# Kernel tuning notes

Hardware: AMD Instinct MI355X
Metric: run time of the kernel (lower is better)

The kernel has to match this reference:

```python
import jax, jax.numpy as jnp
import numpy as np

B, I, T = 8192, 128, 21
H1, H2, H3 = 256, 256, 128


def _init(key, shape, fan_in):
    # torch-style uniform(-1/sqrt(fan_in), 1/sqrt(fan_in))
    bound = 1.0 / np.sqrt(fan_in)
    return jax.random.uniform(key, shape, jnp.float32, -bound, bound)


def setup_inputs() -> dict:
    key = jax.random.key(0)
    ks = jax.random.split(key, 16)
    x = jax.random.normal(ks[0], (B, I, T), jnp.float32)
    d = {"x": x}
    # stacked LSTM weights (PyTorch layout: W_ih (4H, in), gate order i,f,g,o)
    d["W1_ih"] = _init(ks[1], (4 * H1, I), H1)
    d["b1_ih"] = _init(ks[2], (4 * H1,), H1)
    d["b1_hh"] = _init(ks[3], (4 * H1,), H1)
    d["W2_ih"] = _init(ks[4], (4 * H2, H1), H2)
    d["b2_ih"] = _init(ks[5], (4 * H2,), H2)
    d["b2_hh"] = _init(ks[6], (4 * H2,), H2)
    d["W3_ih"] = _init(ks[7], (4 * H3, H2), H3)
    d["b3_ih"] = _init(ks[8], (4 * H3,), H3)
    d["b3_hh"] = _init(ks[9], (4 * H3,), H3)
    d["fc1_w"] = _init(ks[10], (1, H3), H3)
    d["fc1_b"] = _init(ks[11], (1,), H3)
    d["fc2_w"] = _init(ks[12], (T, T), T)
    d["fc2_b"] = _init(ks[13], (T,), T)
    return d


def _lstm_cell_step(xt, W_ih, b_ih, b_hh):
    # single timestep with h0 = c0 = 0, so the W_hh @ h0 term vanishes
    gates = xt @ W_ih.T + (b_ih + b_hh)          # (B, 21, 4H)
    i, f, g, o = jnp.split(gates, 4, axis=-1)    # torch gate order i,f,g,o
    c = jax.nn.sigmoid(i) * jnp.tanh(g)          # f * c0 = 0
    return jax.nn.sigmoid(o) * jnp.tanh(c)


def reference(x, W1_ih, b1_ih, b1_hh, W2_ih, b2_ih, b2_hh,
              W3_ih, b3_ih, b3_hh, fc1_w, fc1_b, fc2_w, fc2_b):
    # fold the 21 independent single-step columns into the batch dim
    xt = jnp.transpose(x, (0, 2, 1))             # (B, 21, I)
    h1 = _lstm_cell_step(xt, W1_ih, b1_ih, b1_hh)   # (B, 21, H1)
    h2 = _lstm_cell_step(h1, W2_ih, b2_ih, b2_hh)   # (B, 21, H2)
    h3 = _lstm_cell_step(h2, W3_ih, b3_ih, b3_hh)   # (B, 21, H3)
    y = h3 @ fc1_w.T + fc1_b                     # (B, 21, 1)
    y = y[..., 0][:, None, :]                    # (B, 1, 21)  == x_torch
    out = y @ fc2_w.T + fc2_b                    # (B, 1, 21)
    return out
```

## Files before the change

### kernel.cpp

```cpp
#include <hip/hip_runtime.h>
#include <hip/hip_bf16.h>
#include <stdint.h>


typedef __attribute__((ext_vector_type(8))) short bf16x8;
typedef __attribute__((ext_vector_type(4))) float f32x4;

#define M_ROWS 172032
#define BATCH  8192

__device__ __forceinline__ float bf2f(unsigned short u) {
    union { unsigned int i; float f; } v; v.i = ((unsigned int)u) << 16; return v.f;
}
__device__ __forceinline__ unsigned short f2bf(float f) {
    union { float f; unsigned int i; } v; v.f = f;
    unsigned int r = v.i + 0x7fffu + ((v.i >> 16) & 1u);
    return (unsigned short)(r >> 16);
}
__device__ __forceinline__ float sigmoidf_(float x) {
    return __builtin_amdgcn_rcpf(1.0f + __expf(-x));
}
__device__ __forceinline__ float tanhf_(float x) {
    x = fminf(fmaxf(x, -20.0f), 20.0f);
    float e = __expf(-2.0f * x);
    return (1.0f - e) * __builtin_amdgcn_rcpf(1.0f + e);
}

__global__ __launch_bounds__(256) void k_convert(
    const float* __restrict__ src, unsigned short* __restrict__ dst, int n4)
{
    int i = blockIdx.x * 256 + threadIdx.x;
    if (i < n4) {
        float4 v = ((const float4*)src)[i];
        ushort4 o;
        o.x = f2bf(v.x); o.y = f2bf(v.y); o.z = f2bf(v.z); o.w = f2bf(v.w);
        ((ushort4*)dst)[i] = o;
    }
}

__global__ __launch_bounds__(256) void k_transpose(
    const float* __restrict__ x, unsigned short* __restrict__ xt)
{
    __shared__ unsigned short tile[128 * 22];
    const int b = blockIdx.x, tid = threadIdx.x;
    const float* xb = x + (size_t)b * 2688;
    for (int idx = tid; idx < 2688; idx += 256) {
        int i = idx / 21, t = idx - i * 21;
        tile[i * 22 + t] = f2bf(xb[idx]);
    }
    __syncthreads();
    unsigned short* xtb = xt + (size_t)b * 2688;
    for (int idx = tid; idx < 2688; idx += 256) {
        int t = idx >> 7, i = idx & 127;
        xtb[t * 128 + i] = tile[i * 22 + t];
    }
}

template<int K, int HG>
__global__ __launch_bounds__(256, 2) void k_gemm_act(
    const unsigned short* __restrict__ A,
    const unsigned short* __restrict__ W,
    const float* __restrict__ bih,
    const float* __restrict__ bhh,
    unsigned short* __restrict__ Hout)
{
    __shared__ __align__(16) unsigned short As[128 * 64];
    __shared__ __align__(16) unsigned short Ws[192 * 64];
    __shared__ float Bs[192];

    const int tid  = threadIdx.x;
    const int wave = tid >> 6;
    const int lane = tid & 63;
    const int wm = wave >> 1;
    const int wn = wave & 1;
    const int r0 = blockIdx.x * 128;
    const int c0 = blockIdx.y * 64;

    if (tid < 192) {
        int g = tid >> 6, c = tid & 63;
        int gbase = (g == 0) ? 0 : (g + 1) * HG;
        int idx = gbase + c0 + c;
        Bs[tid] = bih[idx] + bhh[idx];
    }

    f32x4 acc[3][4][2];
#pragma unroll
    for (int g = 0; g < 3; ++g)
#pragma unroll
        for (int m = 0; m < 4; ++m)
#pragma unroll
            for (int n = 0; n < 2; ++n)
                acc[g][m][n] = (f32x4){0.f, 0.f, 0.f, 0.f};

#pragma unroll
    for (int kk = 0; kk < K; kk += 64) {
        bf16x8 av[4], wv[6];
#pragma unroll
        for (int i = 0; i < 4; ++i) {
            int q = tid + 256 * i;
            int row = q >> 3, off = (q & 7) * 8;
            av[i] = *(const bf16x8*)(A + (size_t)(r0 + row) * K + kk + off);
        }
#pragma unroll
        for (int i = 0; i < 6; ++i) {
            int q = tid + 256 * i;
            int lrow = q >> 3, off = (q & 7) * 8;
            int gate = lrow >> 6, n = lrow & 63;
            int gbase = (gate == 0) ? 0 : (gate + 1) * HG;
            wv[i] = *(const bf16x8*)(W + (size_t)(gbase + c0 + n) * K + kk + off);
        }
        if (kk) __syncthreads();
#pragma unroll
        for (int i = 0; i < 4; ++i) {
            int q = tid + 256 * i;
            int row = q >> 3, slot = (q & 7) ^ (row & 7);
            *(bf16x8*)&As[row * 64 + slot * 8] = av[i];
        }
#pragma unroll
        for (int i = 0; i < 6; ++i) {
            int q = tid + 256 * i;
            int row = q >> 3, slot = (q & 7) ^ (row & 7);
            *(bf16x8*)&Ws[row * 64 + slot * 8] = wv[i];
        }
        __syncthreads();

#pragma unroll
        for (int ks = 0; ks < 64; ks += 32) {
            bf16x8 af[4];
            bf16x8 bfr[3][2];
            const int rsel = lane & 15;
            const int slot = (ks >> 3) | (lane >> 4);
            const int soff = (slot ^ (rsel & 7)) * 8;
#pragma unroll
            for (int m = 0; m < 4; ++m)
                af[m] = *(const bf16x8*)&As[(wm * 64 + m * 16 + rsel) * 64 + soff];
#pragma unroll
            for (int g = 0; g < 3; ++g)
#pragma unroll
                for (int n = 0; n < 2; ++n)
                    bfr[g][n] = *(const bf16x8*)&Ws[(g * 64 + wn * 32 + n * 16 + rsel) * 64 + soff];
#pragma unroll
            for (int g = 0; g < 3; ++g)
#pragma unroll
                for (int m = 0; m < 4; ++m)
#pragma unroll
                    for (int n = 0; n < 2; ++n)
                        acc[g][m][n] = __builtin_amdgcn_mfma_f32_16x16x32_bf16(
                            af[m], bfr[g][n], acc[g][m][n], 0, 0, 0);
        }
    }

    const int quad = lane >> 4;
    const int csel = lane & 15;
#pragma unroll
    for (int m = 0; m < 4; ++m) {
#pragma unroll
        for (int n = 0; n < 2; ++n) {
            int cloc = wn * 32 + n * 16 + csel;
            float bi = Bs[cloc], bg = Bs[64 + cloc], bo = Bs[128 + cloc];
            f32x4 vi = acc[0][m][n], vg = acc[1][m][n], vo = acc[2][m][n];
#pragma unroll
            for (int r = 0; r < 4; ++r) {
                int row = r0 + wm * 64 + m * 16 + quad * 4 + r;
                float cv = sigmoidf_(vi[r] + bi) * tanhf_(vg[r] + bg);
                float h  = sigmoidf_(vo[r] + bo) * tanhf_(cv);
                Hout[(size_t)row * HG + c0 + cloc] = f2bf(h);
            }
        }
    }
}

#define FSTR 169
__global__ __launch_bounds__(256) void k_final(
    const unsigned short* __restrict__ h3,
    const float* __restrict__ fc1w,
    const float* __restrict__ fc1b,
    const float* __restrict__ fc2w,
    const float* __restrict__ fc2b,
    float* __restrict__ out)
{
    __shared__ unsigned short ht[128 * FSTR];
    __shared__ float fwl[128];
    __shared__ float yl[168];
    __shared__ float f2l[441];
    __shared__ float f2bl[21];

    const int tid = threadIdx.x;
    const int b0 = blockIdx.x * 8;

    if (tid < 128) fwl[tid] = fc1w[tid];
    for (int i = tid; i < 441; i += 256) f2l[i] = fc2w[i];
    if (tid < 21) f2bl[tid] = fc2b[tid];

    const unsigned int* hsrc = (const unsigned int*)(h3 + (size_t)b0 * 2688);
    for (int gi = tid; gi < 10752; gi += 256) {
        unsigned int v = hsrc[gi];
        int e = gi * 2;
        int task = e >> 7;
        int c = e & 127;
        ht[c * FSTR + task] = (unsigned short)(v & 0xffffu);
        ht[(c + 1) * FSTR + task] = (unsigned short)(v >> 16);
    }
    __syncthreads();

    const float f1b = fc1b[0];
    if (tid < 168) {
        float s = f1b;
#pragma unroll 8
        for (int c = 0; c < 128; ++c)
            s += fwl[c] * bf2f(ht[c * FSTR + tid]);
        yl[tid] = s;
    }
    __syncthreads();
    if (tid < 168) {
        int bloc = tid / 21;
        int tp = tid - bloc * 21;
        float s = f2bl[tp];
#pragma unroll
        for (int t = 0; t < 21; ++t)
            s += yl[bloc * 21 + t] * f2l[tp * 21 + t];
        out[(size_t)(b0 + bloc) * 21 + tp] = s;
    }
}

extern "C" void kernel_launch(void* const* d_in, const int* in_sizes, int n_in,
                              void* d_out, int out_size, void* d_ws, size_t ws_size,
                              hipStream_t stream)
{
    const float* x    = (const float*)d_in[0];
    const float* W1   = (const float*)d_in[1];
    const float* b1i  = (const float*)d_in[2];
    const float* b1h  = (const float*)d_in[3];
    const float* W2   = (const float*)d_in[4];
    const float* b2i  = (const float*)d_in[5];
    const float* b2h  = (const float*)d_in[6];
    const float* W3   = (const float*)d_in[7];
    const float* b3i  = (const float*)d_in[8];
    const float* b3h  = (const float*)d_in[9];
    const float* fc1w = (const float*)d_in[10];
    const float* fc1b = (const float*)d_in[11];
    const float* fc2w = (const float*)d_in[12];
    const float* fc2b = (const float*)d_in[13];
    float* out = (float*)d_out;

    unsigned short* Wc1 = (unsigned short*)d_ws;
    unsigned short* Wc2 = Wc1 + 131072;
    unsigned short* Wc3 = Wc2 + 262144;
    unsigned short* buf = Wc3 + 131072;

    int C = 1;
    while (C < 64 && 1048576 + (size_t)(M_ROWS / C) * 1536 > ws_size) C <<= 1;
    const int R  = M_ROWS / C;
    const int Bc = BATCH / C;

    unsigned short* xt = buf;
    unsigned short* h1 = xt + (size_t)R * 128;
    unsigned short* h2 = h1 + (size_t)R * 256;
    unsigned short* h3 = h2 + (size_t)R * 256;

    k_convert<<<128, 256, 0, stream>>>(W1, Wc1, 32768);
    k_convert<<<256, 256, 0, stream>>>(W2, Wc2, 65536);
    k_convert<<<128, 256, 0, stream>>>(W3, Wc3, 32768);

    for (int c = 0; c < C; ++c) {
        const float* xc = x + (size_t)c * Bc * 2688;
        k_transpose<<<Bc, 256, 0, stream>>>(xc, xt);
        k_gemm_act<128, 256><<<dim3(R / 128, 4), 256, 0, stream>>>(xt, Wc1, b1i, b1h, h1);
        k_gemm_act<256, 256><<<dim3(R / 128, 4), 256, 0, stream>>>(h1, Wc2, b2i, b2h, h2);
        k_gemm_act<256, 128><<<dim3(R / 128, 2), 256, 0, stream>>>(h2, Wc3, b3i, b3h, h3);
        k_final<<<Bc / 8, 256, 0, stream>>>(h3, fc1w, fc1b, fc2w, fc2b,
                                            out + (size_t)c * Bc * 21);
    }
}
```

Measured before the change: 421.5 us.

## Load GEMM tiles directly into LDS via global_load_lds and swap grid order

```diff
diff --git a/kernel.cpp b/kernel.cpp
--- a/kernel.cpp
+++ b/kernel.cpp
@@ -24,6 +24,13 @@
     x = fminf(fmaxf(x, -20.0f), 20.0f);
     float e = __expf(-2.0f * x);
     return (1.0f - e) * __builtin_amdgcn_rcpf(1.0f + e);
+}
+
+__device__ __forceinline__ void gload_lds16(const unsigned short* g, unsigned short* l) {
+    __builtin_amdgcn_global_load_lds(
+        (const __attribute__((address_space(1))) unsigned int*)g,
+        (__attribute__((address_space(3))) unsigned int*)l,
+        16, 0, 0);
 }
 
 __global__ __launch_bounds__(256) void k_convert(
@@ -57,7 +64,7 @@
 }
 
 template<int K, int HG>
-__global__ __launch_bounds__(256, 2) void k_gemm_act(
+__global__ __launch_bounds__(256, 3) void k_gemm_act(
     const unsigned short* __restrict__ A,
     const unsigned short* __restrict__ W,
     const float* __restrict__ bih,
@@ -73,8 +80,27 @@
     const int lane = tid & 63;
     const int wm = wave >> 1;
     const int wn = wave & 1;
-    const int r0 = blockIdx.x * 128;
-    const int c0 = blockIdx.y * 64;
+    const int c0 = blockIdx.x * 64;
+    const int r0 = blockIdx.y * 128;
+
+    const unsigned short* aptr[4];
+#pragma unroll
+    for (int i = 0; i < 4; ++i) {
+        int q16 = (wave * 4 + i) * 64 + lane;
+        int row = q16 >> 3, pslot = q16 & 7;
+        int lslot = pslot ^ (row & 7);
+        aptr[i] = A + (size_t)(r0 + row) * K + lslot * 8;
+    }
+    const unsigned short* wptr[6];
+#pragma unroll
+    for (int i = 0; i < 6; ++i) {
+        int q16 = (wave * 6 + i) * 64 + lane;
+        int lrow = q16 >> 3, pslot = q16 & 7;
+        int lslot = pslot ^ (lrow & 7);
+        int gate = lrow >> 6, n = lrow & 63;
+        int gbase = (gate == 0) ? 0 : (gate + 1) * HG;
+        wptr[i] = W + (size_t)(gbase + c0 + n) * K + lslot * 8;
+    }
 
     if (tid < 192) {
         int g = tid >> 6, c = tid & 63;
@@ -94,34 +120,13 @@
 
 #pragma unroll
     for (int kk = 0; kk < K; kk += 64) {
-        bf16x8 av[4], wv[6];
-#pragma unroll
-        for (int i = 0; i < 4; ++i) {
-            int q = tid + 256 * i;
-            int row = q >> 3, off = (q & 7) * 8;
-            av[i] = *(const bf16x8*)(A + (size_t)(r0 + row) * K + kk + off);
-        }
-#pragma unroll
-        for (int i = 0; i < 6; ++i) {
-            int q = tid + 256 * i;
-            int lrow = q >> 3, off = (q & 7) * 8;
-            int gate = lrow >> 6, n = lrow & 63;
-            int gbase = (gate == 0) ? 0 : (gate + 1) * HG;
-            wv[i] = *(const bf16x8*)(W + (size_t)(gbase + c0 + n) * K + kk + off);
-        }
         if (kk) __syncthreads();
 #pragma unroll
-        for (int i = 0; i < 4; ++i) {
-            int q = tid + 256 * i;
-            int row = q >> 3, slot = (q & 7) ^ (row & 7);
-            *(bf16x8*)&As[row * 64 + slot * 8] = av[i];
-        }
-#pragma unroll
-        for (int i = 0; i < 6; ++i) {
-            int q = tid + 256 * i;
-            int row = q >> 3, slot = (q & 7) ^ (row & 7);
-            *(bf16x8*)&Ws[row * 64 + slot * 8] = wv[i];
-        }
+        for (int i = 0; i < 4; ++i)
+            gload_lds16(aptr[i] + kk, &As[(wave * 4 + i) * 512]);
+#pragma unroll
+        for (int i = 0; i < 6; ++i)
+            gload_lds16(wptr[i] + kk, &Ws[(wave * 6 + i) * 512]);
         __syncthreads();
 
 #pragma unroll
@@ -265,9 +270,9 @@
     for (int c = 0; c < C; ++c) {
         const float* xc = x + (size_t)c * Bc * 2688;
         k_transpose<<<Bc, 256, 0, stream>>>(xc, xt);
-        k_gemm_act<128, 256><<<dim3(R / 128, 4), 256, 0, stream>>>(xt, Wc1, b1i, b1h, h1);
-        k_gemm_act<256, 256><<<dim3(R / 128, 4), 256, 0, stream>>>(h1, Wc2, b2i, b2h, h2);
-        k_gemm_act<256, 128><<<dim3(R / 128, 2), 256, 0, stream>>>(h2, Wc3, b3i, b3h, h3);
+        k_gemm_act<128, 256><<<dim3(4, R / 128), 256, 0, stream>>>(xt, Wc1, b1i, b1h, h1);
+        k_gemm_act<256, 256><<<dim3(4, R / 128), 256, 0, stream>>>(h1, Wc2, b2i, b2h, h2);
+        k_gemm_act<256, 128><<<dim3(2, R / 128), 256, 0, stream>>>(h2, Wc3, b3i, b3h, h3);
         k_final<<<Bc / 8, 256, 0, stream>>>(h3, fc1w, fc1b, fc2w, fc2b,
                                             out + (size_t)c * Bc * 21);
     }
```

Result: slower. 435.6 us (+3.3%).
